# Kernel optimization log

Hardware: AMD Instinct MI355X
Metric: run time of the kernel (lower is better)

The kernel has to match this reference:

```python
import jax, jax.numpy as jnp
import numpy as np

INPUT_DIM = 512
HIDDEN_DIM = 512
T = 16384


def setup_inputs() -> dict:
    key = jax.random.key(0)
    ks = jax.random.split(key, 9)
    s_in = 1.0 / np.sqrt(INPUT_DIM)
    s_h = 1.0 / np.sqrt(HIDDEN_DIM)
    u = lambda k, shape, s: jax.random.uniform(k, shape, jnp.float32, -s, s)
    return {
        "inputs": jax.random.normal(ks[0], (T, INPUT_DIM), jnp.float32),
        # encoder Linear(input_dim -> hidden_dim)
        "enc_w": u(ks[1], (HIDDEN_DIM, INPUT_DIM), s_in),
        "enc_b": u(ks[2], (HIDDEN_DIM,), s_in),
        # GRUCell(hidden_dim, hidden_dim): weight_ih [3H,H], weight_hh [3H,H], bias [3H], bias_n [H]
        "w_ih": u(ks[3], (3 * HIDDEN_DIM, HIDDEN_DIM), s_h),
        "w_hh": u(ks[4], (3 * HIDDEN_DIM, HIDDEN_DIM), s_h),
        "b_ih": u(ks[5], (3 * HIDDEN_DIM,), s_h),
        "b_n": u(ks[6], (HIDDEN_DIM,), s_h),
        # decoder Linear(hidden_dim -> input_dim)
        "dec_w": u(ks[7], (INPUT_DIM, HIDDEN_DIM), s_h),
        "dec_b": u(ks[8], (INPUT_DIM,), s_h),
    }


def reference(inputs, enc_w, enc_b, w_ih, w_hh, b_ih, b_n, dec_w, dec_b):
    H = w_hh.shape[1]
    # Encoder and the input-side GRU gates depend only on x_t -> batch them as one big GEMM.
    emb = inputs @ enc_w.T + enc_b              # [T, H]
    igates = emb @ w_ih.T + b_ih                # [T, 3H] = (ir, iz, in) per step

    def step(h, ig):
        ir, iz, inn = jnp.split(ig, 3)
        hr, hz, hn = jnp.split(w_hh @ h, 3)
        r = jax.nn.sigmoid(ir + hr)             # reset gate
        z = jax.nn.sigmoid(iz + hz)             # update gate (equinox: 'inp')
        n = jnp.tanh(inn + r * (hn + b_n))      # candidate, bias_n inside reset product
        h_new = n + z * (h - n)
        return h_new, h_new

    h0 = jnp.zeros((H,), inputs.dtype)
    _, hs = jax.lax.scan(step, h0, igates)      # [T, H]
    preds = hs @ dec_w.T + dec_b                # decoder applied to every step's hidden
    return preds
```

## Files before the change

kernel.cpp:

```cpp
#include <hip/hip_runtime.h>
#include <hip/hip_bf16.h>
#include <cstdint>
#include <cstddef>

#define T_STEPS 16384
#define HID 512
#define NSLOTS 32
#define NLAUNCH 256
#define ESC_ITERS 1024

typedef float f32x4 __attribute__((ext_vector_type(4)));
typedef float f32x2 __attribute__((ext_vector_type(2)));

__device__ __forceinline__ float wave_reduce_sum(float x) {
#define DPP_ADD(ctrl)                                                          \
  x += __int_as_float(__builtin_amdgcn_update_dpp(                             \
      0, __float_as_int(x), (ctrl), 0xF, 0xF, true))
  DPP_ADD(0x111);
  DPP_ADD(0x112);
  DPP_ADD(0x114);
  DPP_ADD(0x118);
  DPP_ADD(0x142);
  DPP_ADD(0x143);
#undef DPP_ADD
  return x;
}

__device__ __forceinline__ float fsigmoid(float x) {
  return __builtin_amdgcn_rcpf(1.f + __expf(-x));
}
__device__ __forceinline__ float ftanh(float x) {
  return 1.f - 2.f * __builtin_amdgcn_rcpf(1.f + __expf(2.f * x));
}

__device__ __forceinline__ void poll_near(const float* a, f32x4& x, f32x4& y) {
  f32x4 u, v;
  asm volatile(
      "global_load_dwordx4 %0, %[p], off sc0\n\t"
      "global_load_dwordx4 %1, %[p], off offset:1024 sc0\n\t"
      "s_waitcnt vmcnt(0)"
      : "=&v"(u), "=&v"(v) : [p] "v"(a) : "memory");
  x = u; y = v;
}
__device__ __forceinline__ void poll_far(const float* a, f32x4& x, f32x4& y) {
  f32x4 u, v;
  asm volatile(
      "global_load_dwordx4 %0, %[p], off sc0 sc1\n\t"
      "global_load_dwordx4 %1, %[p], off offset:1024 sc0 sc1\n\t"
      "s_waitcnt vmcnt(0)"
      : "=&v"(u), "=&v"(v) : [p] "v"(a) : "memory");
  x = u; y = v;
}

__global__ void k_prep(float* __restrict__ hsz, float* __restrict__ bc,
                       int* __restrict__ ctrl,
                       const float* __restrict__ w_ih,
                       const float* __restrict__ enc_b,
                       const float* __restrict__ b_ih) {
  const int gid = blockIdx.x * blockDim.x + threadIdx.x;
  const int gsz = gridDim.x * blockDim.x;
  float4* h4 = reinterpret_cast<float4*>(hsz);
  const float4 zer = make_float4(0.f, 0.f, 0.f, 0.f);
  const float4 sen = make_float4(2.f, 2.f, 2.f, 2.f);
  const int n4 = (T_STEPS + 1) * HID / 4;
  for (int i = gid; i < n4; i += gsz) h4[i] = (i < HID / 4) ? zer : sen;
  if (gid == 0) ctrl[0] = 0;
  if (gid >= 1 && gid < 1 + NLAUNCH) ctrl[gid] = -1;
  if (gid >= 1 + NLAUNCH && gid < 1 + 2 * NLAUNCH) ctrl[gid] = -2;
  if (gid < 3 * HID) {
    float acc = b_ih[gid];
    const float* wr = w_ih + (size_t)gid * HID;
    for (int j = 0; j < HID; ++j) acc = fmaf(wr[j], enc_b[j], acc);
    bc[gid] = acc;
  }
}

__global__ void k_transpose512(const float* __restrict__ in, float* __restrict__ out) {
  __shared__ float tile[32][33];
  const int bx = blockIdx.x * 32, by = blockIdx.y * 32;
  const int x = threadIdx.x, y = threadIdx.y;
#pragma unroll
  for (int i = 0; i < 32; i += 8) tile[y + i][x] = in[(size_t)(by + y + i) * 512 + bx + x];
  __syncthreads();
#pragma unroll
  for (int i = 0; i < 32; i += 8) out[(size_t)(bx + y + i) * 512 + by + x] = tile[x][y + i];
}

template <bool ADD_BIAS, bool OUT_BF16>
__global__ __launch_bounds__(256) void k_gemm_bt(
    const float* __restrict__ A, const float* __restrict__ B,
    const float* __restrict__ bias, void* __restrict__ C,
    int M, int N, int K) {
  __shared__ float As[16][68];
  __shared__ float Bs[16][68];
  const int n0 = blockIdx.x * 64;
  const int m0 = blockIdx.y * 64;
  const int tid = (int)threadIdx.x;
  const int tx = tid & 15, ty = tid >> 4;
  const int lr = tid >> 2;
  const int lc = (tid & 3) * 4;

  float acc[4][4] = {};
  for (int k0 = 0; k0 < K; k0 += 16) {
    const float4 a4 = *reinterpret_cast<const float4*>(A + (size_t)(m0 + lr) * K + k0 + lc);
    const float4 b4 = *reinterpret_cast<const float4*>(B + (size_t)(n0 + lr) * K + k0 + lc);
    __syncthreads();
    As[lc + 0][lr] = a4.x; As[lc + 1][lr] = a4.y; As[lc + 2][lr] = a4.z; As[lc + 3][lr] = a4.w;
    Bs[lc + 0][lr] = b4.x; Bs[lc + 1][lr] = b4.y; Bs[lc + 2][lr] = b4.z; Bs[lc + 3][lr] = b4.w;
    __syncthreads();
#pragma unroll
    for (int kk = 0; kk < 16; ++kk) {
      const float4 av = *reinterpret_cast<const float4*>(&As[kk][ty * 4]);
      const float4 bv = *reinterpret_cast<const float4*>(&Bs[kk][tx * 4]);
      const float a[4] = {av.x, av.y, av.z, av.w};
      const float b[4] = {bv.x, bv.y, bv.z, bv.w};
#pragma unroll
      for (int i = 0; i < 4; ++i)
#pragma unroll
        for (int j = 0; j < 4; ++j) acc[i][j] = fmaf(a[i], b[j], acc[i][j]);
    }
  }

  float bv[4] = {0.f, 0.f, 0.f, 0.f};
  if (ADD_BIAS) {
#pragma unroll
    for (int j = 0; j < 4; ++j) bv[j] = bias[n0 + tx * 4 + j];
  }
#pragma unroll
  for (int i = 0; i < 4; ++i) {
    const int m = m0 + ty * 4 + i;
    if (OUT_BF16) {
      __hip_bfloat16* Cb = (__hip_bfloat16*)C;
#pragma unroll
      for (int j = 0; j < 4; ++j)
        Cb[(size_t)m * N + n0 + tx * 4 + j] = __float2bfloat16(acc[i][j] + bv[j]);
    } else {
      float4 v;
      v.x = acc[i][0] + bv[0]; v.y = acc[i][1] + bv[1];
      v.z = acc[i][2] + bv[2]; v.w = acc[i][3] + bv[3];
      *reinterpret_cast<float4*>((float*)C + (size_t)m * N + n0 + tx * 4) = v;
    }
  }
}

template <bool XL>
__device__ void scan_loop(int slot, int wv, int lane,
                          const float* __restrict__ w_hh,
                          const uint32_t* __restrict__ ig32,
                          const float* __restrict__ b_n,
                          float* __restrict__ hsz,
                          float* lds_h, float* gather) {
  const int e0 = slot * 16 + 2 * wv;

  f32x4 wA[6], wB[6];
#pragma unroll
  for (int i = 0; i < 6; ++i) {
    const float* wrow = w_hh + (size_t)((i >> 1) * HID + e0 + (i & 1)) * HID;
#pragma unroll
    for (int c = 0; c < 4; ++c) {
      wA[i][c] = wrow[4 * lane + c];
      wB[i][c] = wrow[256 + 4 * lane + c];
    }
  }

  float bn0 = 0.f, bn1 = 0.f, h0 = 0.f, h1 = 0.f;
  if (lane == 63) { bn0 = b_n[e0]; bn1 = b_n[e0 + 1]; }

  uint32_t gAr = 0, gAz = 0, gAn = 0, gBr = 0, gBz = 0, gBn = 0;
  if (lane == 63) {
    const uint32_t* r0 = ig32 + (e0 >> 1);
    gAr = r0[0]; gAz = r0[256]; gAn = r0[512];
    const uint32_t* r1 = r0 + 768;
    gBr = r1[0]; gBz = r1[256]; gBn = r1[512];
  }

  bool esc = false;

#pragma unroll 1
  for (int t = 0; t < T_STEPS; ++t) {
    asm volatile("" : "+v"(wA[0]), "+v"(wA[1]), "+v"(wA[2]), "+v"(wA[3]),
                      "+v"(wA[4]), "+v"(wA[5]), "+v"(wB[0]), "+v"(wB[1]),
                      "+v"(wB[2]), "+v"(wB[3]), "+v"(wB[4]), "+v"(wB[5]));

    if (wv == 0) {
      f32x4 hva = {0.f, 0.f, 0.f, 0.f}, hvb = {0.f, 0.f, 0.f, 0.f};
      if (t > 0) {
        const float* p = hsz + (size_t)t * HID + 4 * lane;
        hva = (f32x4)2.f; hvb = (f32x4)2.f;
        int iters = 0;
        for (;;) {
          f32x4 ta, tb;
          if (XL && !esc) poll_near(p, ta, tb); else poll_far(p, ta, tb);
#pragma unroll
          for (int c = 0; c < 4; ++c) {
            hva[c] = (hva[c] < 1.5f) ? hva[c] : ta[c];
            hvb[c] = (hvb[c] < 1.5f) ? hvb[c] : tb[c];
          }
          bool ok = (hva[0] < 1.5f) & (hva[1] < 1.5f) & (hva[2] < 1.5f) &
                    (hva[3] < 1.5f) & (hvb[0] < 1.5f) & (hvb[1] < 1.5f) &
                    (hvb[2] < 1.5f) & (hvb[3] < 1.5f);
          if (__all(ok)) break;
          ++iters;
          if (iters > 1) __builtin_amdgcn_s_sleep(1);
          if (XL && !esc && iters > ESC_ITERS) {
            esc = true;
            if (lane < 16) {
              float rv = gather[lane];
              float* rd = hsz + (size_t)t * HID + slot * 16 + lane;
              asm volatile("global_store_dword %0, %1, off sc0 sc1"
                           :: "v"(rd), "v"(rv) : "memory");
            }
          }
        }
      }
      *reinterpret_cast<f32x4*>(&lds_h[4 * lane]) = hva;
      *reinterpret_cast<f32x4*>(&lds_h[256 + 4 * lane]) = hvb;
    }
    __syncthreads();

    if (wv == 1 && t + 2 <= T_STEPS) {
      const float* pf = hsz + (size_t)(t + 2) * HID + 4 * lane;
      f32x4 d1 = *reinterpret_cast<const f32x4*>(pf);
      f32x4 d2 = *reinterpret_cast<const f32x4*>(pf + 256);
      asm volatile("" :: "v"(d1), "v"(d2));
    }

    const f32x4 hva = *reinterpret_cast<const f32x4*>(&lds_h[4 * lane]);
    const f32x4 hvb = *reinterpret_cast<const f32x4*>(&lds_h[256 + 4 * lane]);

    uint32_t gCr = 0, gCz = 0, gCn = 0;
    if (lane == 63) {
      const int tn = (t + 2 < T_STEPS) ? t + 2 : T_STEPS - 1;
      const uint32_t* rn = ig32 + (size_t)tn * 768 + (e0 >> 1);
      gCr = rn[0]; gCz = rn[256]; gCn = rn[512];
    }

    float s0, s1, s2, s3, s4, s5;
    {
      float a;
#define ROWDOT(i, dst)                                                         \
      a = 0.f;                                                                 \
      a = fmaf(wA[i][0], hva[0], a); a = fmaf(wA[i][1], hva[1], a);            \
      a = fmaf(wA[i][2], hva[2], a); a = fmaf(wA[i][3], hva[3], a);            \
      a = fmaf(wB[i][0], hvb[0], a); a = fmaf(wB[i][1], hvb[1], a);            \
      a = fmaf(wB[i][2], hvb[2], a); a = fmaf(wB[i][3], hvb[3], a);            \
      dst = wave_reduce_sum(a)
      ROWDOT(0, s0); ROWDOT(1, s1); ROWDOT(2, s2);
      ROWDOT(3, s3); ROWDOT(4, s4); ROWDOT(5, s5);
#undef ROWDOT
    }

    if (lane == 63) {
      const float ir0 = __uint_as_float(gAr << 16);
      const float ir1 = __uint_as_float(gAr & 0xffff0000u);
      const float iz0 = __uint_as_float(gAz << 16);
      const float iz1 = __uint_as_float(gAz & 0xffff0000u);
      const float in0 = __uint_as_float(gAn << 16);
      const float in1 = __uint_as_float(gAn & 0xffff0000u);

      const float r0 = fsigmoid(ir0 + s0);
      const float r1 = fsigmoid(ir1 + s1);
      const float z0 = fsigmoid(iz0 + s2);
      const float z1 = fsigmoid(iz1 + s3);
      const float n0 = ftanh(in0 + r0 * (s4 + bn0));
      const float n1 = ftanh(in1 + r1 * (s5 + bn1));
      h0 = n0 + z0 * (h0 - n0);
      h1 = n1 + z1 * (h1 - n1);
      *reinterpret_cast<f32x2*>(&gather[2 * wv]) = (f32x2){h0, h1};
    }
    __syncthreads();

    if (wv == 0 && lane < 16) {
      const float v = gather[lane];
      float* dst = hsz + (size_t)(t + 1) * HID + slot * 16 + lane;
      if (XL && !esc)
        asm volatile("global_store_dword %0, %1, off sc0"
                     :: "v"(dst), "v"(v) : "memory");
      else
        asm volatile("global_store_dword %0, %1, off sc0 sc1"
                     :: "v"(dst), "v"(v) : "memory");
    }

    gAr = gBr; gAz = gBz; gAn = gBn;
    gBr = gCr; gBz = gCz; gBn = gCn;
  }
}

__global__ __launch_bounds__(512) void k_scan(
    const float* __restrict__ w_hh, const __hip_bfloat16* __restrict__ igb,
    const float* __restrict__ b_n, float* __restrict__ hsz,
    int* __restrict__ ctrl) {
  int* counter = ctrl;
  int* census  = ctrl + 1;
  int* assign  = ctrl + 1 + NLAUNCH;
  __shared__ int s_assign;
  __shared__ float lds_h[HID];
  __shared__ float gather[16];

  int myxcc;
  asm("s_getreg_b32 %0, hwreg(HW_REG_XCC_ID)" : "=s"(myxcc));
  const int bid = (int)blockIdx.x;

  if (threadIdx.x == 0) {
    __hip_atomic_store(&census[bid], myxcc, __ATOMIC_RELAXED,
                       __HIP_MEMORY_SCOPE_AGENT);
    __hip_atomic_fetch_add(counter, 1, __ATOMIC_RELEASE,
                           __HIP_MEMORY_SCOPE_AGENT);
    if (bid == 0) {
      const uint64_t t0 = __builtin_amdgcn_s_memrealtime();
      int cnt;
      for (;;) {
        cnt = __hip_atomic_load(counter, __ATOMIC_ACQUIRE,
                                __HIP_MEMORY_SCOPE_AGENT);
        if (cnt >= NLAUNCH) break;
        if (cnt >= NSLOTS &&
            (__builtin_amdgcn_s_memrealtime() - t0) > 20000) break;
        __builtin_amdgcn_s_sleep(1);
      }
      int hist[8] = {0, 0, 0, 0, 0, 0, 0, 0};
      for (int i = 0; i < NLAUNCH; ++i) {
        int c = __hip_atomic_load(&census[i], __ATOMIC_RELAXED,
                                  __HIP_MEMORY_SCOPE_AGENT);
        if (c >= 0 && c < 8) ++hist[c];
      }
      int pick = -1;
      for (int x = 0; x < 8; ++x)
        if (pick < 0 && hist[x] >= NSLOTS) pick = x;
      const int mode = (pick >= 0) ? 1 : 0;
      int slot = 0;
      for (int i = 0; i < NLAUNCH; ++i) {
        int c = __hip_atomic_load(&census[i], __ATOMIC_RELAXED,
                                  __HIP_MEMORY_SCOPE_AGENT);
        int a = -1;
        const bool take = (pick >= 0) ? (c == pick) : (c >= 0);
        if (take && slot < NSLOTS) { a = slot * 2 + mode; ++slot; }
        __hip_atomic_store(&assign[i], a, __ATOMIC_RELAXED,
                           __HIP_MEMORY_SCOPE_AGENT);
      }
    }
    int a;
    do {
      a = __hip_atomic_load(&assign[bid], __ATOMIC_ACQUIRE,
                            __HIP_MEMORY_SCOPE_AGENT);
      if (a == -2) __builtin_amdgcn_s_sleep(1);
    } while (a == -2);
    s_assign = a;
  }
  __syncthreads();
  const int a = s_assign;
  if (a < 0) return;
  const int slot = a >> 1, mode = a & 1;

  const int wv = (int)threadIdx.x >> 6;
  const int lane = (int)threadIdx.x & 63;
  const uint32_t* ig32 = reinterpret_cast<const uint32_t*>(igb);

  if (mode) scan_loop<true>(slot, wv, lane, w_hh, ig32, b_n, hsz, lds_h, gather);
  else      scan_loop<false>(slot, wv, lane, w_hh, ig32, b_n, hsz, lds_h, gather);
}

extern "C" void kernel_launch(void* const* d_in, const int* in_sizes, int n_in,
                              void* d_out, int out_size, void* d_ws, size_t ws_size,
                              hipStream_t stream) {
  (void)in_sizes; (void)n_in; (void)out_size; (void)ws_size;
  const float* x     = (const float*)d_in[0];
  const float* enc_w = (const float*)d_in[1];
  const float* enc_b = (const float*)d_in[2];
  const float* w_ih  = (const float*)d_in[3];
  const float* w_hh  = (const float*)d_in[4];
  const float* b_ih  = (const float*)d_in[5];
  const float* b_n   = (const float*)d_in[6];
  const float* dec_w = (const float*)d_in[7];
  const float* dec_b = (const float*)d_in[8];
  float* out = (float*)d_out;

  uintptr_t p = (uintptr_t)d_ws;
  auto carve = [&](size_t bytes) {
    void* r = (void*)p;
    p += (bytes + 255) & ~(size_t)255;
    return r;
  };
  int* ctrl           = (int*)carve((size_t)(1 + 2 * NLAUNCH) * 4);
  float* encwT        = (float*)carve((size_t)512 * 512 * 4);
  float* Wc           = (float*)carve((size_t)1536 * 512 * 4);
  float* bc           = (float*)carve((size_t)1536 * 4);
  __hip_bfloat16* igb = (__hip_bfloat16*)carve((size_t)T_STEPS * 1536 * 2);
  float* hsz          = (float*)carve((size_t)(T_STEPS + 1) * HID * 4);

  k_prep<<<1024, 256, 0, stream>>>(hsz, bc, ctrl, w_ih, enc_b, b_ih);
  k_transpose512<<<dim3(16, 16), dim3(32, 8), 0, stream>>>(enc_w, encwT);
  k_gemm_bt<false, false><<<dim3(512 / 64, 1536 / 64), 256, 0, stream>>>(
      w_ih, encwT, nullptr, Wc, 1536, 512, 512);
  k_gemm_bt<true, true><<<dim3(1536 / 64, 16384 / 64), 256, 0, stream>>>(
      x, Wc, bc, igb, T_STEPS, 1536, 512);
  k_scan<<<NLAUNCH, 512, 0, stream>>>(w_hh, igb, b_n, hsz, ctrl);
  k_gemm_bt<true, false><<<dim3(512 / 64, 16384 / 64), 256, 0, stream>>>(
      hsz + HID, dec_w, dec_b, out, T_STEPS, 512, 512);
}
```

Measured before the change: 25.19 ms.

## Poll compact per-slot ready flags before reading hidden-state rows in scan

Adds a per-step array of 32 int flags, one per block slot, that each producer sets after its hidden-state store drains. Consumers first poll the small 128-byte flag line and read the full 2KB hidden row only once every slot has reported, instead of repeatedly loading the whole row and checking sentinel values. The prefetch now warms the flag line for step t+2 instead of the hidden row. The escape path from near-cache to far-coherence polling also changes: it triggers later, republishes the last few rows, and then alternates near and far polls. This adds an extra store plus a vmcnt wait per step on the critical path, which may offset the cheaper polling.

```diff
diff --git a/kernel.cpp b/kernel.cpp
--- a/kernel.cpp
+++ b/kernel.cpp
@@ -7,7 +7,7 @@
 #define HID 512
 #define NSLOTS 32
 #define NLAUNCH 256
-#define ESC_ITERS 1024
+#define ESC_ITERS 16384
 
 typedef float f32x4 __attribute__((ext_vector_type(4)));
 typedef float f32x2 __attribute__((ext_vector_type(2)));
@@ -51,9 +51,39 @@
       : "=&v"(u), "=&v"(v) : [p] "v"(a) : "memory");
   x = u; y = v;
 }
+__device__ __forceinline__ int ldflag_near(const int* a) {
+  int v;
+  asm volatile("global_load_dword %0, %1, off sc0\n\ts_waitcnt vmcnt(0)"
+               : "=v"(v) : "v"(a) : "memory");
+  return v;
+}
+__device__ __forceinline__ int ldflag_far(const int* a) {
+  int v;
+  asm volatile("global_load_dword %0, %1, off sc0 sc1\n\ts_waitcnt vmcnt(0)"
+               : "=v"(v) : "v"(a) : "memory");
+  return v;
+}
+__device__ __forceinline__ float ld_near(const float* a) {
+  float v;
+  asm volatile("global_load_dword %0, %1, off sc0\n\ts_waitcnt vmcnt(0)"
+               : "=v"(v) : "v"(a) : "memory");
+  return v;
+}
+__device__ __forceinline__ void st_near_f(float* a, float v) {
+  asm volatile("global_store_dword %0, %1, off sc0" :: "v"(a), "v"(v) : "memory");
+}
+__device__ __forceinline__ void st_far_f(float* a, float v) {
+  asm volatile("global_store_dword %0, %1, off sc0 sc1" :: "v"(a), "v"(v) : "memory");
+}
+__device__ __forceinline__ void st_near_i(int* a, int v) {
+  asm volatile("global_store_dword %0, %1, off sc0" :: "v"(a), "v"(v) : "memory");
+}
+__device__ __forceinline__ void st_far_i(int* a, int v) {
+  asm volatile("global_store_dword %0, %1, off sc0 sc1" :: "v"(a), "v"(v) : "memory");
+}
 
 __global__ void k_prep(float* __restrict__ hsz, float* __restrict__ bc,
-                       int* __restrict__ ctrl,
+                       int* __restrict__ ctrl, int* __restrict__ cnt,
                        const float* __restrict__ w_ih,
                        const float* __restrict__ enc_b,
                        const float* __restrict__ b_ih) {
@@ -64,6 +94,8 @@
   const float4 sen = make_float4(2.f, 2.f, 2.f, 2.f);
   const int n4 = (T_STEPS + 1) * HID / 4;
   for (int i = gid; i < n4; i += gsz) h4[i] = (i < HID / 4) ? zer : sen;
+  const int nf = (T_STEPS + 1) * 32;
+  for (int i = gid; i < nf; i += gsz) cnt[i] = 0;
   if (gid == 0) ctrl[0] = 0;
   if (gid >= 1 && gid < 1 + NLAUNCH) ctrl[gid] = -1;
   if (gid >= 1 + NLAUNCH && gid < 1 + 2 * NLAUNCH) ctrl[gid] = -2;
@@ -148,7 +180,7 @@
                           const float* __restrict__ w_hh,
                           const uint32_t* __restrict__ ig32,
                           const float* __restrict__ b_n,
-                          float* __restrict__ hsz,
+                          float* __restrict__ hsz, int* __restrict__ cnt,
                           float* lds_h, float* gather) {
   const int e0 = slot * 16 + 2 * wv;
 
@@ -185,31 +217,58 @@
     if (wv == 0) {
       f32x4 hva = {0.f, 0.f, 0.f, 0.f}, hvb = {0.f, 0.f, 0.f, 0.f};
       if (t > 0) {
-        const float* p = hsz + (size_t)t * HID + 4 * lane;
+        const float* rowp = hsz + (size_t)t * HID + 4 * lane;
+        const int* fl = cnt + (size_t)t * 32 + lane;
         hva = (f32x4)2.f; hvb = (f32x4)2.f;
         int iters = 0;
         for (;;) {
-          f32x4 ta, tb;
-          if (XL && !esc) poll_near(p, ta, tb); else poll_far(p, ta, tb);
-#pragma unroll
-          for (int c = 0; c < 4; ++c) {
-            hva[c] = (hva[c] < 1.5f) ? hva[c] : ta[c];
-            hvb[c] = (hvb[c] < 1.5f) ? hvb[c] : tb[c];
-          }
-          bool ok = (hva[0] < 1.5f) & (hva[1] < 1.5f) & (hva[2] < 1.5f) &
-                    (hva[3] < 1.5f) & (hvb[0] < 1.5f) & (hvb[1] < 1.5f) &
-                    (hvb[2] < 1.5f) & (hvb[3] < 1.5f);
-          if (__all(ok)) break;
-          ++iters;
-          if (iters > 1) __builtin_amdgcn_s_sleep(1);
-          if (XL && !esc && iters > ESC_ITERS) {
-            esc = true;
-            if (lane < 16) {
-              float rv = gather[lane];
-              float* rd = hsz + (size_t)t * HID + slot * 16 + lane;
-              asm volatile("global_store_dword %0, %1, off sc0 sc1"
-                           :: "v"(rd), "v"(rv) : "memory");
+          bool done = false;
+          if (XL && !esc) {
+            int f = 1;
+            if (lane < 32) f = ldflag_near(fl);
+            if (__all(f != 0)) {
+              poll_near(rowp, hva, hvb);
+              done = (hva[0] < 1.5f) & (hva[1] < 1.5f) & (hva[2] < 1.5f) &
+                     (hva[3] < 1.5f) & (hvb[0] < 1.5f) & (hvb[1] < 1.5f) &
+                     (hvb[2] < 1.5f) & (hvb[3] < 1.5f);
             }
+            if (__all(done)) break;
+            ++iters;
+            if (iters > ESC_ITERS) {
+              esc = true;
+              if (lane < 16) {
+                const int r0 = (t > 4) ? t - 3 : 1;
+                for (int r = r0; r <= t; ++r) {
+                  float* q = hsz + (size_t)r * HID + slot * 16 + lane;
+                  const float v = ld_near(q);
+                  if (v < 1.5f) st_far_f(q, v);
+                }
+              }
+              hva = (f32x4)2.f; hvb = (f32x4)2.f;
+            }
+          } else if (XL) {
+            f32x4 ta, tb;
+            if (iters & 1) poll_far(rowp, ta, tb); else poll_near(rowp, ta, tb);
+#pragma unroll
+            for (int c = 0; c < 4; ++c) {
+              hva[c] = (hva[c] < 1.5f) ? hva[c] : ta[c];
+              hvb[c] = (hvb[c] < 1.5f) ? hvb[c] : tb[c];
+            }
+            done = (hva[0] < 1.5f) & (hva[1] < 1.5f) & (hva[2] < 1.5f) &
+                   (hva[3] < 1.5f) & (hvb[0] < 1.5f) & (hvb[1] < 1.5f) &
+                   (hvb[2] < 1.5f) & (hvb[3] < 1.5f);
+            if (__all(done)) break;
+            ++iters;
+          } else {
+            int f = 1;
+            if (lane < 32) f = ldflag_far(fl);
+            if (__all(f != 0)) {
+              poll_far(rowp, hva, hvb);
+              done = (hva[0] < 1.5f) & (hva[1] < 1.5f) & (hva[2] < 1.5f) &
+                     (hva[3] < 1.5f) & (hvb[0] < 1.5f) & (hvb[1] < 1.5f) &
+                     (hvb[2] < 1.5f) & (hvb[3] < 1.5f);
+            }
+            if (__all(done)) break;
           }
         }
       }
@@ -218,15 +277,13 @@
     }
     __syncthreads();
 
-    if (wv == 1 && t + 2 <= T_STEPS) {
-      const float* pf = hsz + (size_t)(t + 2) * HID + 4 * lane;
-      f32x4 d1 = *reinterpret_cast<const f32x4*>(pf);
-      f32x4 d2 = *reinterpret_cast<const f32x4*>(pf + 256);
-      asm volatile("" :: "v"(d1), "v"(d2));
-    }
-
     const f32x4 hva = *reinterpret_cast<const f32x4*>(&lds_h[4 * lane]);
     const f32x4 hvb = *reinterpret_cast<const f32x4*>(&lds_h[256 + 4 * lane]);
+
+    if (wv == 1 && lane < 32 && t + 2 <= T_STEPS) {
+      const int d = cnt[(size_t)(t + 2) * 32 + lane];
+      asm volatile("" :: "v"(d));
+    }
 
     uint32_t gCr = 0, gCz = 0, gCn = 0;
     if (lane == 63) {
@@ -270,15 +327,27 @@
     }
     __syncthreads();
 
-    if (wv == 0 && lane < 16) {
-      const float v = gather[lane];
-      float* dst = hsz + (size_t)(t + 1) * HID + slot * 16 + lane;
-      if (XL && !esc)
-        asm volatile("global_store_dword %0, %1, off sc0"
-                     :: "v"(dst), "v"(v) : "memory");
-      else
-        asm volatile("global_store_dword %0, %1, off sc0 sc1"
-                     :: "v"(dst), "v"(v) : "memory");
+    if (wv == 0) {
+      if (lane < 16) {
+        const float v = gather[lane];
+        float* dst = hsz + (size_t)(t + 1) * HID + slot * 16 + lane;
+        if (XL) {
+          st_near_f(dst, v);
+          if (esc) st_far_f(dst, v);
+        } else {
+          st_far_f(dst, v);
+        }
+      }
+      asm volatile("s_waitcnt vmcnt(0)" ::: "memory");
+      if (lane == 0) {
+        int* fp = cnt + (size_t)(t + 1) * 32 + slot;
+        if (XL) {
+          st_near_i(fp, 1);
+          if (esc) st_far_i(fp, 1);
+        } else {
+          st_far_i(fp, 1);
+        }
+      }
     }
 
     gAr = gBr; gAz = gBz; gAn = gBn;
@@ -289,7 +358,7 @@
 __global__ __launch_bounds__(512) void k_scan(
     const float* __restrict__ w_hh, const __hip_bfloat16* __restrict__ igb,
     const float* __restrict__ b_n, float* __restrict__ hsz,
-    int* __restrict__ ctrl) {
+    int* __restrict__ cnt, int* __restrict__ ctrl) {
   int* counter = ctrl;
   int* census  = ctrl + 1;
   int* assign  = ctrl + 1 + NLAUNCH;
@@ -308,12 +377,12 @@
                            __HIP_MEMORY_SCOPE_AGENT);
     if (bid == 0) {
       const uint64_t t0 = __builtin_amdgcn_s_memrealtime();
-      int cnt;
+      int cnt_;
       for (;;) {
-        cnt = __hip_atomic_load(counter, __ATOMIC_ACQUIRE,
-                                __HIP_MEMORY_SCOPE_AGENT);
-        if (cnt >= NLAUNCH) break;
-        if (cnt >= NSLOTS &&
+        cnt_ = __hip_atomic_load(counter, __ATOMIC_ACQUIRE,
+                                 __HIP_MEMORY_SCOPE_AGENT);
+        if (cnt_ >= NLAUNCH) break;
+        if (cnt_ >= NSLOTS &&
             (__builtin_amdgcn_s_memrealtime() - t0) > 20000) break;
         __builtin_amdgcn_s_sleep(1);
       }
@@ -355,8 +424,10 @@
   const int lane = (int)threadIdx.x & 63;
   const uint32_t* ig32 = reinterpret_cast<const uint32_t*>(igb);
 
-  if (mode) scan_loop<true>(slot, wv, lane, w_hh, ig32, b_n, hsz, lds_h, gather);
-  else      scan_loop<false>(slot, wv, lane, w_hh, ig32, b_n, hsz, lds_h, gather);
+  if (mode)
+    scan_loop<true>(slot, wv, lane, w_hh, ig32, b_n, hsz, cnt, lds_h, gather);
+  else
+    scan_loop<false>(slot, wv, lane, w_hh, ig32, b_n, hsz, cnt, lds_h, gather);
 }
 
 extern "C" void kernel_launch(void* const* d_in, const int* in_sizes, int n_in,
@@ -381,19 +452,20 @@
     return r;
   };
   int* ctrl           = (int*)carve((size_t)(1 + 2 * NLAUNCH) * 4);
+  int* cnt            = (int*)carve((size_t)(T_STEPS + 1) * 32 * 4);
   float* encwT        = (float*)carve((size_t)512 * 512 * 4);
   float* Wc           = (float*)carve((size_t)1536 * 512 * 4);
   float* bc           = (float*)carve((size_t)1536 * 4);
   __hip_bfloat16* igb = (__hip_bfloat16*)carve((size_t)T_STEPS * 1536 * 2);
   float* hsz          = (float*)carve((size_t)(T_STEPS + 1) * HID * 4);
 
-  k_prep<<<1024, 256, 0, stream>>>(hsz, bc, ctrl, w_ih, enc_b, b_ih);
+  k_prep<<<1024, 256, 0, stream>>>(hsz, bc, ctrl, cnt, w_ih, enc_b, b_ih);
   k_transpose512<<<dim3(16, 16), dim3(32, 8), 0, stream>>>(enc_w, encwT);
   k_gemm_bt<false, false><<<dim3(512 / 64, 1536 / 64), 256, 0, stream>>>(
       w_ih, encwT, nullptr, Wc, 1536, 512, 512);
   k_gemm_bt<true, true><<<dim3(1536 / 64, 16384 / 64), 256, 0, stream>>>(
       x, Wc, bc, igb, T_STEPS, 1536, 512);
-  k_scan<<<NLAUNCH, 512, 0, stream>>>(w_hh, igb, b_n, hsz, ctrl);
+  k_scan<<<NLAUNCH, 512, 0, stream>>>(w_hh, igb, b_n, hsz, cnt, ctrl);
   k_gemm_bt<true, false><<<dim3(512 / 64, 16384 / 64), 256, 0, stream>>>(
       hsz + HID, dec_w, dec_b, out, T_STEPS, 512, 512);
 }
```

Result: slower. 37.20 ms (+47.6%).

## Poll one sentinel word per slot before reading full hidden row

Applied to the files above, without the earlier changes.

The wait for step t's hidden state now first polls one word per producer slot (32 lanes) until every slot has written, and only then reads the full 512-float row with vector loads. The escalation path is reworked: its threshold is raised, it alternates near and far cache-scoped loads, it republishes the last few rows with far scope, and after escalation each store goes out with both near and far scope. The aim is lighter polling traffic and a more robust cross-XCD visibility fallback, at the cost of an extra load phase and double stores once escalated.

```diff
diff --git a/kernel.cpp b/kernel.cpp
--- a/kernel.cpp
+++ b/kernel.cpp
@@ -7,7 +7,7 @@
 #define HID 512
 #define NSLOTS 32
 #define NLAUNCH 256
-#define ESC_ITERS 1024
+#define ESC_ITERS 4096
 
 typedef float f32x4 __attribute__((ext_vector_type(4)));
 typedef float f32x2 __attribute__((ext_vector_type(2)));
@@ -50,6 +50,24 @@
       "s_waitcnt vmcnt(0)"
       : "=&v"(u), "=&v"(v) : [p] "v"(a) : "memory");
   x = u; y = v;
+}
+__device__ __forceinline__ float ld_near(const float* a) {
+  float v;
+  asm volatile("global_load_dword %0, %1, off sc0\n\ts_waitcnt vmcnt(0)"
+               : "=v"(v) : "v"(a) : "memory");
+  return v;
+}
+__device__ __forceinline__ float ld_far(const float* a) {
+  float v;
+  asm volatile("global_load_dword %0, %1, off sc0 sc1\n\ts_waitcnt vmcnt(0)"
+               : "=v"(v) : "v"(a) : "memory");
+  return v;
+}
+__device__ __forceinline__ void st_near_f(float* a, float v) {
+  asm volatile("global_store_dword %0, %1, off sc0" :: "v"(a), "v"(v) : "memory");
+}
+__device__ __forceinline__ void st_far_f(float* a, float v) {
+  asm volatile("global_store_dword %0, %1, off sc0 sc1" :: "v"(a), "v"(v) : "memory");
 }
 
 __global__ void k_prep(float* __restrict__ hsz, float* __restrict__ bc,
@@ -185,12 +203,34 @@
     if (wv == 0) {
       f32x4 hva = {0.f, 0.f, 0.f, 0.f}, hvb = {0.f, 0.f, 0.f, 0.f};
       if (t > 0) {
-        const float* p = hsz + (size_t)t * HID + 4 * lane;
-        hva = (f32x4)2.f; hvb = (f32x4)2.f;
+        const float* rowp = hsz + (size_t)t * HID + 4 * lane;
+        const float* gatep = hsz + (size_t)t * HID + 16 * (lane & 31);
         int iters = 0;
         for (;;) {
+          float g = 0.f;
+          const bool nearpass = XL && (!esc || ((iters & 1) == 0));
+          if (lane < 32) g = nearpass ? ld_near(gatep) : ld_far(gatep);
+          if (__all(g < 1.5f)) break;
+          ++iters;
+          if (iters > 1) __builtin_amdgcn_s_sleep(1);
+          if (XL && !esc && iters > ESC_ITERS) {
+            esc = true;
+            if (lane < 16) {
+              const int r0 = (t > 4) ? t - 3 : 1;
+              for (int r = r0; r <= t; ++r) {
+                float* q = hsz + (size_t)r * HID + slot * 16 + lane;
+                const float v = ld_near(q);
+                if (v < 1.5f) st_far_f(q, v);
+              }
+            }
+          }
+        }
+        hva = (f32x4)2.f; hvb = (f32x4)2.f;
+        int it2 = 0;
+        for (;;) {
           f32x4 ta, tb;
-          if (XL && !esc) poll_near(p, ta, tb); else poll_far(p, ta, tb);
+          const bool np = XL && (!esc || ((it2 & 1) == 0));
+          if (np) poll_near(rowp, ta, tb); else poll_far(rowp, ta, tb);
 #pragma unroll
           for (int c = 0; c < 4; ++c) {
             hva[c] = (hva[c] < 1.5f) ? hva[c] : ta[c];
@@ -200,23 +240,16 @@
                     (hva[3] < 1.5f) & (hvb[0] < 1.5f) & (hvb[1] < 1.5f) &
                     (hvb[2] < 1.5f) & (hvb[3] < 1.5f);
           if (__all(ok)) break;
-          ++iters;
-          if (iters > 1) __builtin_amdgcn_s_sleep(1);
-          if (XL && !esc && iters > ESC_ITERS) {
-            esc = true;
-            if (lane < 16) {
-              float rv = gather[lane];
-              float* rd = hsz + (size_t)t * HID + slot * 16 + lane;
-              asm volatile("global_store_dword %0, %1, off sc0 sc1"
-                           :: "v"(rd), "v"(rv) : "memory");
-            }
-          }
+          ++it2;
         }
       }
       *reinterpret_cast<f32x4*>(&lds_h[4 * lane]) = hva;
       *reinterpret_cast<f32x4*>(&lds_h[256 + 4 * lane]) = hvb;
     }
     __syncthreads();
+
+    const f32x4 hva = *reinterpret_cast<const f32x4*>(&lds_h[4 * lane]);
+    const f32x4 hvb = *reinterpret_cast<const f32x4*>(&lds_h[256 + 4 * lane]);
 
     if (wv == 1 && t + 2 <= T_STEPS) {
       const float* pf = hsz + (size_t)(t + 2) * HID + 4 * lane;
@@ -224,9 +257,6 @@
       f32x4 d2 = *reinterpret_cast<const f32x4*>(pf + 256);
       asm volatile("" :: "v"(d1), "v"(d2));
     }
-
-    const f32x4 hva = *reinterpret_cast<const f32x4*>(&lds_h[4 * lane]);
-    const f32x4 hvb = *reinterpret_cast<const f32x4*>(&lds_h[256 + 4 * lane]);
 
     uint32_t gCr = 0, gCz = 0, gCn = 0;
     if (lane == 63) {
@@ -273,12 +303,12 @@
     if (wv == 0 && lane < 16) {
       const float v = gather[lane];
       float* dst = hsz + (size_t)(t + 1) * HID + slot * 16 + lane;
-      if (XL && !esc)
-        asm volatile("global_store_dword %0, %1, off sc0"
-                     :: "v"(dst), "v"(v) : "memory");
-      else
-        asm volatile("global_store_dword %0, %1, off sc0 sc1"
-                     :: "v"(dst), "v"(v) : "memory");
+      if (XL) {
+        st_near_f(dst, v);
+        if (esc) st_far_f(dst, v);
+      } else {
+        st_far_f(dst, v);
+      }
     }
 
     gAr = gBr; gAz = gBz; gAn = gBn;
@@ -355,8 +385,10 @@
   const int lane = (int)threadIdx.x & 63;
   const uint32_t* ig32 = reinterpret_cast<const uint32_t*>(igb);
 
-  if (mode) scan_loop<true>(slot, wv, lane, w_hh, ig32, b_n, hsz, lds_h, gather);
-  else      scan_loop<false>(slot, wv, lane, w_hh, ig32, b_n, hsz, lds_h, gather);
+  if (mode)
+    scan_loop<true>(slot, wv, lane, w_hh, ig32, b_n, hsz, lds_h, gather);
+  else
+    scan_loop<false>(slot, wv, lane, w_hh, ig32, b_n, hsz, lds_h, gather);
 }
 
 extern "C" void kernel_launch(void* const* d_in, const int* in_sizes, int n_in,
```

Measured after the change: 33.61 ms. 33.4% more time.
